# Kernel optimization log

Hardware: AMD Instinct MI355X
Metric: run time of the kernel (lower is better)

The kernel has to match this reference:

```python
import jax, jax.numpy as jnp
import numpy as np


def setup_inputs() -> dict:
    key = jax.random.key(0)
    k1, k2, k3 = jax.random.split(key, 3)
    Na, Nb, D, K = 1024, 1024, 512, 256
    a = jax.random.normal(k1, (Na, D), dtype=jnp.float32)
    b = jax.random.normal(k2, (Nb, D), dtype=jnp.float32)
    feats = jax.random.normal(k3, (K, D), dtype=jnp.float32)
    return {"a": a, "b": b, "feats": feats}


def reference(a, b, feats):
    # 'ignorematch' mode of the Difference module.
    # Project both sets onto the feature bank: [Na,K] and [Nb,K]
    a_fk = jnp.matmul(a, feats.T)          # [Na, K]
    b_fk = jnp.matmul(b, feats.T)          # [Nb, K]
    a_e = a_fk[:, None, :]                 # [Na, 1, K]
    b_e = b_fk[None, :, :]                 # [1, Nb, K]
    # features present in a (>0) but absent in b (<=0)
    mask = ((a_e > 0) & (b_e <= 0)).astype(a_fk.dtype)  # [Na, Nb, K]
    result = jnp.sum(a_e * mask, axis=2)   # [Na, Nb]
    return result
```

## Files before the change

### kernel.cpp

```cpp
#include <hip/hip_runtime.h>


#define BM 64
#define BN 64
#define BK 32
#define PAD 4

__global__ __launch_bounds__(256) void gemm_af_kernel(
    const float* __restrict__ a, const float* __restrict__ b,
    const float* __restrict__ feats, float* __restrict__ p, float* __restrict__ msk)
{
    const int num_n = 256 / BN;
    const int bm = blockIdx.x / num_n;
    const int bn = blockIdx.x % num_n;
    const int m0 = bm * BM;
    const int n0 = bn * BN;

    const float* X;
    float* Out;
    bool is_a;
    if (m0 < 1024) { X = a + (size_t)m0 * 512; Out = p   + (size_t)m0        * 256; is_a = true;  }
    else           { X = b + (size_t)(m0 - 1024) * 512; Out = msk + (size_t)(m0 - 1024) * 256; is_a = false; }

    __shared__ float Xs[BK][BM + PAD];
    __shared__ float Fs[BK][BN + PAD];

    const int tid = threadIdx.x;
    const int tm = tid / 16;
    const int tn = tid % 16;

    float acc[4][4];
    #pragma unroll
    for (int i = 0; i < 4; i++)
        #pragma unroll
        for (int j = 0; j < 4; j++) acc[i][j] = 0.f;

    for (int k0 = 0; k0 < 512; k0 += BK) {
        #pragma unroll
        for (int r = 0; r < 2; r++) {
            int idx = tid + r * 256;
            int lm  = idx >> 3;
            int lk  = (idx & 7) * 4;
            float4 v = *(const float4*)(X + lm * 512 + k0 + lk);
            Xs[lk + 0][lm] = v.x; Xs[lk + 1][lm] = v.y;
            Xs[lk + 2][lm] = v.z; Xs[lk + 3][lm] = v.w;
        }
        #pragma unroll
        for (int r = 0; r < 2; r++) {
            int idx = tid + r * 256;
            int ln  = idx >> 3;
            int lk  = (idx & 7) * 4;
            float4 v = *(const float4*)(feats + (size_t)(n0 + ln) * 512 + k0 + lk);
            Fs[lk + 0][ln] = v.x; Fs[lk + 1][ln] = v.y;
            Fs[lk + 2][ln] = v.z; Fs[lk + 3][ln] = v.w;
        }
        __syncthreads();

        #pragma unroll
        for (int kk = 0; kk < BK; kk++) {
            float xv[4], fv[4];
            #pragma unroll
            for (int i = 0; i < 4; i++) xv[i] = Xs[kk][tm * 4 + i];
            #pragma unroll
            for (int j = 0; j < 4; j++) fv[j] = Fs[kk][tn * 4 + j];
            #pragma unroll
            for (int i = 0; i < 4; i++)
                #pragma unroll
                for (int j = 0; j < 4; j++)
                    acc[i][j] += xv[i] * fv[j];
        }
        __syncthreads();
    }

    #pragma unroll
    for (int i = 0; i < 4; i++) {
        int row = tm * 4 + i;
        #pragma unroll
        for (int j = 0; j < 4; j++) {
            int col = n0 + tn * 4 + j;
            float v = acc[i][j];
            float o = is_a ? (v > 0.f ? v : 0.f) : (v <= 0.f ? 1.f : 0.f);
            Out[row * 256 + col] = o;
        }
    }
}

__global__ __launch_bounds__(256) void gemm_pm_kernel(
    const float* __restrict__ p, const float* __restrict__ msk,
    float* __restrict__ out)
{
    const int bi = blockIdx.x / 16;
    const int bj = blockIdx.x % 16;
    const int i0 = bi * BM;
    const int j0 = bj * BN;

    __shared__ float Ps[BK][BM + PAD];
    __shared__ float Ms[BK][BN + PAD];

    const int tid = threadIdx.x;
    const int tm = tid / 16;
    const int tn = tid % 16;

    float acc[4][4];
    #pragma unroll
    for (int i = 0; i < 4; i++)
        #pragma unroll
        for (int j = 0; j < 4; j++) acc[i][j] = 0.f;

    for (int k0 = 0; k0 < 256; k0 += BK) {
        #pragma unroll
        for (int r = 0; r < 2; r++) {
            int idx = tid + r * 256;
            int li  = idx >> 3;
            int lk  = (idx & 7) * 4;
            float4 v = *(const float4*)(p + (size_t)(i0 + li) * 256 + k0 + lk);
            Ps[lk + 0][li] = v.x; Ps[lk + 1][li] = v.y;
            Ps[lk + 2][li] = v.z; Ps[lk + 3][li] = v.w;
        }
        #pragma unroll
        for (int r = 0; r < 2; r++) {
            int idx = tid + r * 256;
            int lj  = idx >> 3;
            int lk  = (idx & 7) * 4;
            float4 v = *(const float4*)(msk + (size_t)(j0 + lj) * 256 + k0 + lk);
            Ms[lk + 0][lj] = v.x; Ms[lk + 1][lj] = v.y;
            Ms[lk + 2][lj] = v.z; Ms[lk + 3][lj] = v.w;
        }
        __syncthreads();

        #pragma unroll
        for (int kk = 0; kk < BK; kk++) {
            float pv[4], mv[4];
            #pragma unroll
            for (int i = 0; i < 4; i++) pv[i] = Ps[kk][tm * 4 + i];
            #pragma unroll
            for (int j = 0; j < 4; j++) mv[j] = Ms[kk][tn * 4 + j];
            #pragma unroll
            for (int i = 0; i < 4; i++)
                #pragma unroll
                for (int j = 0; j < 4; j++)
                    acc[i][j] += pv[i] * mv[j];
        }
        __syncthreads();
    }

    #pragma unroll
    for (int i = 0; i < 4; i++) {
        int row = i0 + tm * 4 + i;
        #pragma unroll
        for (int j = 0; j < 4; j++) {
            int col = j0 + tn * 4 + j;
            out[(size_t)row * 1024 + col] = acc[i][j];
        }
    }
}

extern "C" void kernel_launch(void* const* d_in, const int* in_sizes, int n_in,
                              void* d_out, int out_size, void* d_ws, size_t ws_size,
                              hipStream_t stream) {
    const float* a     = (const float*)d_in[0];
    const float* b     = (const float*)d_in[1];
    const float* feats = (const float*)d_in[2];
    float* out = (float*)d_out;
    float* p   = (float*)d_ws;
    float* msk = p + 1024 * 256;

    gemm_af_kernel<<<128, 256, 0, stream>>>(a, b, feats, p, msk);
    gemm_pm_kernel<<<256, 256, 0, stream>>>(p, msk, out);
}
```

Baseline: 95.12 us.

## Split-K first GEMM, add reduction epilogue, and use bf16 MFMA for second GEMM

```diff
diff --git a/kernel.cpp b/kernel.cpp
--- a/kernel.cpp
+++ b/kernel.cpp
@@ -1,33 +1,36 @@
 #include <hip/hip_runtime.h>
+#include <hip/hip_bf16.h>
 
+
+typedef short bf16x8 __attribute__((ext_vector_type(8)));
+typedef float f32x4  __attribute__((ext_vector_type(4)));
 
 #define BM 64
 #define BN 64
 #define BK 32
 #define PAD 4
 
-__global__ __launch_bounds__(256) void gemm_af_kernel(
+__global__ __launch_bounds__(256) void stage1_kernel(
     const float* __restrict__ a, const float* __restrict__ b,
-    const float* __restrict__ feats, float* __restrict__ p, float* __restrict__ msk)
+    const float* __restrict__ feats, float* __restrict__ part)
 {
-    const int num_n = 256 / BN;
-    const int bm = blockIdx.x / num_n;
-    const int bn = blockIdx.x % num_n;
+    const int tile = blockIdx.x >> 2;
+    const int ks   = blockIdx.x & 3;
+    const int bm = tile >> 2;
+    const int bn = tile & 3;
     const int m0 = bm * BM;
     const int n0 = bn * BN;
 
-    const float* X;
-    float* Out;
-    bool is_a;
-    if (m0 < 1024) { X = a + (size_t)m0 * 512; Out = p   + (size_t)m0        * 256; is_a = true;  }
-    else           { X = b + (size_t)(m0 - 1024) * 512; Out = msk + (size_t)(m0 - 1024) * 256; is_a = false; }
+    const float* X = (m0 < 1024) ? (a + (size_t)m0 * 512)
+                                 : (b + (size_t)(m0 - 1024) * 512);
+    float* Out = part + (size_t)ks * 2048 * 256 + (size_t)m0 * 256;
 
     __shared__ float Xs[BK][BM + PAD];
     __shared__ float Fs[BK][BN + PAD];
 
     const int tid = threadIdx.x;
-    const int tm = tid / 16;
-    const int tn = tid % 16;
+    const int tm = tid >> 4;
+    const int tn = tid & 15;
 
     float acc[4][4];
     #pragma unroll
@@ -35,13 +38,15 @@
         #pragma unroll
         for (int j = 0; j < 4; j++) acc[i][j] = 0.f;
 
-    for (int k0 = 0; k0 < 512; k0 += BK) {
+    const int kbase = ks * 128;
+    for (int kt = 0; kt < 4; kt++) {
+        const int k0 = kbase + kt * BK;
         #pragma unroll
         for (int r = 0; r < 2; r++) {
             int idx = tid + r * 256;
             int lm  = idx >> 3;
             int lk  = (idx & 7) * 4;
-            float4 v = *(const float4*)(X + lm * 512 + k0 + lk);
+            float4 v = *(const float4*)(X + (size_t)lm * 512 + k0 + lk);
             Xs[lk + 0][lm] = v.x; Xs[lk + 1][lm] = v.y;
             Xs[lk + 2][lm] = v.z; Xs[lk + 3][lm] = v.w;
         }
@@ -78,80 +83,87 @@
         #pragma unroll
         for (int j = 0; j < 4; j++) {
             int col = n0 + tn * 4 + j;
-            float v = acc[i][j];
-            float o = is_a ? (v > 0.f ? v : 0.f) : (v <= 0.f ? 1.f : 0.f);
-            Out[row * 256 + col] = o;
+            Out[row * 256 + col] = acc[i][j];
         }
     }
 }
 
-__global__ __launch_bounds__(256) void gemm_pm_kernel(
-    const float* __restrict__ p, const float* __restrict__ msk,
+__global__ __launch_bounds__(256) void epilogue_kernel(
+    const float* __restrict__ part,
+    __hip_bfloat16* __restrict__ pbf, __hip_bfloat16* __restrict__ mbf)
+{
+    const int g = blockIdx.x * 256 + threadIdx.x;
+    const int row = g >> 6;
+    const int c4  = (g & 63) * 4;
+
+    const float* base = part + (size_t)row * 256 + c4;
+    float4 s = *(const float4*)base;
+    #pragma unroll
+    for (int sdx = 1; sdx < 4; sdx++) {
+        float4 v = *(const float4*)(base + (size_t)sdx * 2048 * 256);
+        s.x += v.x; s.y += v.y; s.z += v.z; s.w += v.w;
+    }
+
+    if (row < 1024) {
+        __hip_bfloat16* o = pbf + (size_t)row * 256 + c4;
+        o[0] = __float2bfloat16(fmaxf(s.x, 0.f));
+        o[1] = __float2bfloat16(fmaxf(s.y, 0.f));
+        o[2] = __float2bfloat16(fmaxf(s.z, 0.f));
+        o[3] = __float2bfloat16(fmaxf(s.w, 0.f));
+    } else {
+        __hip_bfloat16* o = mbf + (size_t)(row - 1024) * 256 + c4;
+        o[0] = __float2bfloat16(s.x <= 0.f ? 1.f : 0.f);
+        o[1] = __float2bfloat16(s.y <= 0.f ? 1.f : 0.f);
+        o[2] = __float2bfloat16(s.z <= 0.f ? 1.f : 0.f);
+        o[3] = __float2bfloat16(s.w <= 0.f ? 1.f : 0.f);
+    }
+}
+
+__global__ __launch_bounds__(256) void gemm2_kernel(
+    const __hip_bfloat16* __restrict__ p, const __hip_bfloat16* __restrict__ m,
     float* __restrict__ out)
 {
-    const int bi = blockIdx.x / 16;
-    const int bj = blockIdx.x % 16;
-    const int i0 = bi * BM;
-    const int j0 = bj * BN;
+    const int bi = blockIdx.x >> 4;
+    const int bj = blockIdx.x & 15;
+    const int i0 = bi * 32;
+    const int j0 = bj * 64;
 
-    __shared__ float Ps[BK][BM + PAD];
-    __shared__ float Ms[BK][BN + PAD];
+    const int tid  = threadIdx.x;
+    const int w    = tid >> 6;
+    const int lane = tid & 63;
+    const int wi = w >> 1;
+    const int wj = w & 1;
 
-    const int tid = threadIdx.x;
-    const int tm = tid / 16;
-    const int tn = tid % 16;
+    const int l15 = lane & 15;
+    const int q   = lane >> 4;
 
-    float acc[4][4];
+    const int arow  = i0 + wi * 16 + l15;
+    const int jbase = j0 + wj * 32;
+    const int brow0 = jbase + l15;
+    const int brow1 = brow0 + 16;
+
+    const short* ps = (const short*)p;
+    const short* ms = (const short*)m;
+
+    f32x4 acc0 = {0.f, 0.f, 0.f, 0.f};
+    f32x4 acc1 = {0.f, 0.f, 0.f, 0.f};
+
     #pragma unroll
-    for (int i = 0; i < 4; i++)
-        #pragma unroll
-        for (int j = 0; j < 4; j++) acc[i][j] = 0.f;
-
-    for (int k0 = 0; k0 < 256; k0 += BK) {
-        #pragma unroll
-        for (int r = 0; r < 2; r++) {
-            int idx = tid + r * 256;
-            int li  = idx >> 3;
-            int lk  = (idx & 7) * 4;
-            float4 v = *(const float4*)(p + (size_t)(i0 + li) * 256 + k0 + lk);
-            Ps[lk + 0][li] = v.x; Ps[lk + 1][li] = v.y;
-            Ps[lk + 2][li] = v.z; Ps[lk + 3][li] = v.w;
-        }
-        #pragma unroll
-        for (int r = 0; r < 2; r++) {
-            int idx = tid + r * 256;
-            int lj  = idx >> 3;
-            int lk  = (idx & 7) * 4;
-            float4 v = *(const float4*)(msk + (size_t)(j0 + lj) * 256 + k0 + lk);
-            Ms[lk + 0][lj] = v.x; Ms[lk + 1][lj] = v.y;
-            Ms[lk + 2][lj] = v.z; Ms[lk + 3][lj] = v.w;
-        }
-        __syncthreads();
-
-        #pragma unroll
-        for (int kk = 0; kk < BK; kk++) {
-            float pv[4], mv[4];
-            #pragma unroll
-            for (int i = 0; i < 4; i++) pv[i] = Ps[kk][tm * 4 + i];
-            #pragma unroll
-            for (int j = 0; j < 4; j++) mv[j] = Ms[kk][tn * 4 + j];
-            #pragma unroll
-            for (int i = 0; i < 4; i++)
-                #pragma unroll
-                for (int j = 0; j < 4; j++)
-                    acc[i][j] += pv[i] * mv[j];
-        }
-        __syncthreads();
+    for (int k0 = 0; k0 < 256; k0 += 32) {
+        const int ko = k0 + q * 8;
+        bf16x8 av = *(const bf16x8*)(ps + (size_t)arow  * 256 + ko);
+        bf16x8 b0 = *(const bf16x8*)(ms + (size_t)brow0 * 256 + ko);
+        bf16x8 b1 = *(const bf16x8*)(ms + (size_t)brow1 * 256 + ko);
+        acc0 = __builtin_amdgcn_mfma_f32_16x16x32_bf16(av, b0, acc0, 0, 0, 0);
+        acc1 = __builtin_amdgcn_mfma_f32_16x16x32_bf16(av, b1, acc1, 0, 0, 0);
     }
 
+    const int orow = i0 + wi * 16 + q * 4;
+    const int ocol = jbase + l15;
     #pragma unroll
-    for (int i = 0; i < 4; i++) {
-        int row = i0 + tm * 4 + i;
-        #pragma unroll
-        for (int j = 0; j < 4; j++) {
-            int col = j0 + tn * 4 + j;
-            out[(size_t)row * 1024 + col] = acc[i][j];
-        }
+    for (int r = 0; r < 4; r++) {
+        out[(size_t)(orow + r) * 1024 + ocol]      = acc0[r];
+        out[(size_t)(orow + r) * 1024 + ocol + 16] = acc1[r];
     }
 }
 
@@ -162,9 +174,12 @@
     const float* b     = (const float*)d_in[1];
     const float* feats = (const float*)d_in[2];
     float* out = (float*)d_out;
-    float* p   = (float*)d_ws;
-    float* msk = p + 1024 * 256;
 
-    gemm_af_kernel<<<128, 256, 0, stream>>>(a, b, feats, p, msk);
-    gemm_pm_kernel<<<256, 256, 0, stream>>>(p, msk, out);
+    float* part = (float*)d_ws;
+    __hip_bfloat16* pbf = (__hip_bfloat16*)((char*)d_ws + (size_t)8 * 1024 * 1024);
+    __hip_bfloat16* mbf = pbf + 1024 * 256;
+
+    stage1_kernel  <<<512, 256, 0, stream>>>(a, b, feats, part);
+    epilogue_kernel<<<512, 256, 0, stream>>>(part, pbf, mbf);
+    gemm2_kernel   <<<512, 256, 0, stream>>>(pbf, mbf, out);
 }
```

Result: faster. 81.42 us (-14.4%).
